# Performance work log

Measured on AMD Instinct MI355X. Metric: run time of the kernel, lower is better.

Reference implementation:

```python
import jax, jax.numpy as jnp
import numpy as np

NEG = -1000000000.0

def setup_inputs() -> dict:
    key = jax.random.key(0)
    kq, kk, kv = jax.random.split(key, 3)
    B, S, D = 4, 4096, 128
    q = jax.random.normal(kq, (B, S, D), dtype=jnp.float32)
    k = jax.random.normal(kk, (B, S, D), dtype=jnp.float32)
    v = jax.random.normal(kv, (B, S, D), dtype=jnp.float32)
    return {"q": q, "k": k, "v": v, "window_size": 128}

def reference(q, k, v, window_size):
    B, S, D = q.shape
    q = q / jnp.sqrt(jnp.asarray(D, q.dtype))
    # banded mask: keep |i-j| <= window_size-1 (tril(w-1) & triu(-(w-1)))
    idx = jnp.arange(S)
    band = jnp.abs(idx[:, None] - idx[None, :]) <= (window_size - 1)  # [S,S]
    scores = jnp.einsum('bqd,bkd->bqk', q, k)
    scores = jnp.where(band[None, :, :], scores, NEG)
    weights = jax.nn.softmax(scores, axis=-1)
    return jnp.einsum('bqk,bkd->bqd', weights, v)
```

## Files before the change

### kernel.cpp

```cpp
#include <hip/hip_runtime.h>

#define S_LEN  4096
#define D_DIM  128
#define MQ     64
#define KT     64
#define NBATCH 4

#define QS_STR 136
#define KS_STR 136
#define VT_STR 72
#define PS_STR 72

typedef __bf16 bf16x8 __attribute__((ext_vector_type(8)));
typedef float  f32x4  __attribute__((ext_vector_type(4)));
typedef unsigned short u16x4 __attribute__((ext_vector_type(4)));
typedef unsigned short u16x8 __attribute__((ext_vector_type(8)));

__device__ __forceinline__ unsigned short f2bf(float f) {
  unsigned int u = __builtin_bit_cast(unsigned int, f);
  u += 0x7fffu + ((u >> 16) & 1u);
  return (unsigned short)(u >> 16);
}

__device__ __forceinline__ bf16x8 ld8(const unsigned short* p) {
  return __builtin_bit_cast(bf16x8, *(const u16x8*)p);
}

__device__ __forceinline__ f32x4 mfma16(bf16x8 a, bf16x8 b, f32x4 c) {
  return __builtin_amdgcn_mfma_f32_16x16x32_bf16(a, b, c, 0, 0, 0);
}

__global__ __launch_bounds__(256)
void swa_fwd(const float* __restrict__ Qg, const float* __restrict__ Kg,
             const float* __restrict__ Vg, float* __restrict__ Og)
{
  __shared__ __align__(16) unsigned short lds_q[MQ * QS_STR];
  __shared__ __align__(16) unsigned short lds_k[KT * KS_STR];
  __shared__ __align__(16) unsigned short lds_vt[D_DIM * VT_STR];
  __shared__ __align__(16) unsigned short lds_p[4 * 16 * PS_STR];

  const int tid  = threadIdx.x;
  const int b    = blockIdx.x >> 6;
  const int q0   = (blockIdx.x & 63) * MQ;
  const size_t base = (size_t)b * S_LEN * D_DIM;

  const int lane = tid & 63;
  const int wv   = tid >> 6;
  const int quad = lane >> 4;
  const int l15  = lane & 15;

  {
    const float qsc = 1.4426950408889634f * 0.08838834764831845f;
    const float* gq = Qg + base + (size_t)q0 * D_DIM;
#pragma unroll
    for (int j = 0; j < 8; ++j) {
      const int f = j * 1024 + tid * 4;
      const int row = f >> 7, col = f & 127;
      const f32x4 x = *(const f32x4*)(gq + f);
      u16x4 y;
#pragma unroll
      for (int e = 0; e < 4; ++e) y[e] = f2bf(x[e] * qsc);
      *(u16x4*)&lds_q[row * QS_STR + col] = y;
    }
  }
  __syncthreads();

  bf16x8 aq[4];
#pragma unroll
  for (int ks = 0; ks < 4; ++ks)
    aq[ks] = ld8(&lds_q[(wv * 16 + l15) * QS_STR + ks * 32 + quad * 8]);

  float mrow[4], lrow[4];
  f32x4 acc[8];
#pragma unroll
  for (int r = 0; r < 4; ++r) { mrow[r] = -3.0e38f; lrow[r] = 0.0f; }
#pragma unroll
  for (int d = 0; d < 8; ++d) acc[d] = (f32x4){0.f, 0.f, 0.f, 0.f};

  for (int t = 0; t < 5; ++t) {
    const int kb = q0 + (t - 2) * KT;
    if (kb < 0 || kb >= S_LEN) continue;
    __syncthreads();

    {
      const float* gk = Kg + base + (size_t)kb * D_DIM;
#pragma unroll
      for (int j = 0; j < 8; ++j) {
        const int f = j * 1024 + tid * 4;
        const int row = f >> 7, col = f & 127;
        const f32x4 x = *(const f32x4*)(gk + f);
        u16x4 y;
#pragma unroll
        for (int e = 0; e < 4; ++e) y[e] = f2bf(x[e]);
        *(u16x4*)&lds_k[row * KS_STR + col] = y;
      }
    }
    {
      const float* gv = Vg + base + (size_t)kb * D_DIM;
      const int d0 = (tid & 31) * 4;
      const int k0 = (tid >> 5) * 8;
      unsigned short vb[4][8];
#pragma unroll
      for (int kk = 0; kk < 8; ++kk) {
        const f32x4 x = *(const f32x4*)(gv + (size_t)(k0 + kk) * D_DIM + d0);
#pragma unroll
        for (int e = 0; e < 4; ++e) vb[e][kk] = f2bf(x[e]);
      }
#pragma unroll
      for (int e = 0; e < 4; ++e) {
        u16x8 y;
#pragma unroll
        for (int kk = 0; kk < 8; ++kk) y[kk] = vb[e][kk];
        *(u16x8*)&lds_vt[(d0 + e) * VT_STR + k0] = y;
      }
    }
    __syncthreads();

    f32x4 sc[4];
#pragma unroll
    for (int cb = 0; cb < 4; ++cb) {
      f32x4 a = (f32x4){0.f, 0.f, 0.f, 0.f};
#pragma unroll
      for (int ks = 0; ks < 4; ++ks) {
        const bf16x8 kf = ld8(&lds_k[(cb * 16 + l15) * KS_STR + ks * 32 + quad * 8]);
        a = mfma16(aq[ks], kf, a);
      }
      sc[cb] = a;
    }

    if (t == 0 || t == 4) {
      const int off = (t - 2) * KT;
#pragma unroll
      for (int cb = 0; cb < 4; ++cb)
#pragma unroll
        for (int r = 0; r < 4; ++r) {
          const int delta = (wv * 16 + quad * 4 + r) - (off + cb * 16 + l15);
          if (delta > 127 || delta < -127) sc[cb][r] = -1.0e30f;
        }
    }

    float tm[4];
#pragma unroll
    for (int r = 0; r < 4; ++r)
      tm[r] = fmaxf(fmaxf(sc[0][r], sc[1][r]), fmaxf(sc[2][r], sc[3][r]));
#pragma unroll
    for (int r = 0; r < 4; ++r) {
      tm[r] = fmaxf(tm[r], __shfl_xor(tm[r], 1, 64));
      tm[r] = fmaxf(tm[r], __shfl_xor(tm[r], 2, 64));
      tm[r] = fmaxf(tm[r], __shfl_xor(tm[r], 4, 64));
      tm[r] = fmaxf(tm[r], __shfl_xor(tm[r], 8, 64));
    }

    float alpha[4], rs[4];
#pragma unroll
    for (int r = 0; r < 4; ++r) {
      const float mn = fmaxf(mrow[r], tm[r]);
      alpha[r] = exp2f(mrow[r] - mn);
      mrow[r] = mn;
    }
#pragma unroll
    for (int cb = 0; cb < 4; ++cb)
#pragma unroll
      for (int r = 0; r < 4; ++r)
        sc[cb][r] = exp2f(sc[cb][r] - mrow[r]);
#pragma unroll
    for (int r = 0; r < 4; ++r) {
      rs[r] = (sc[0][r] + sc[1][r]) + (sc[2][r] + sc[3][r]);
      rs[r] += __shfl_xor(rs[r], 1, 64);
      rs[r] += __shfl_xor(rs[r], 2, 64);
      rs[r] += __shfl_xor(rs[r], 4, 64);
      rs[r] += __shfl_xor(rs[r], 8, 64);
      lrow[r] = lrow[r] * alpha[r] + rs[r];
    }
#pragma unroll
    for (int d = 0; d < 8; ++d)
#pragma unroll
      for (int r = 0; r < 4; ++r) acc[d][r] *= alpha[r];

    unsigned short* pw = &lds_p[wv * 16 * PS_STR];
#pragma unroll
    for (int cb = 0; cb < 4; ++cb)
#pragma unroll
      for (int r = 0; r < 4; ++r)
        pw[(quad * 4 + r) * PS_STR + cb * 16 + l15] = f2bf(sc[cb][r]);

#pragma unroll
    for (int ks2 = 0; ks2 < 2; ++ks2) {
      const bf16x8 pf = ld8(&pw[l15 * PS_STR + ks2 * 32 + quad * 8]);
#pragma unroll
      for (int d = 0; d < 8; ++d) {
        const bf16x8 vf = ld8(&lds_vt[(d * 16 + l15) * VT_STR + ks2 * 32 + quad * 8]);
        acc[d] = mfma16(pf, vf, acc[d]);
      }
    }
  }

  float inv[4];
#pragma unroll
  for (int r = 0; r < 4; ++r) inv[r] = 1.0f / lrow[r];
  float* go = Og + base + (size_t)q0 * D_DIM;
#pragma unroll
  for (int d = 0; d < 8; ++d)
#pragma unroll
    for (int r = 0; r < 4; ++r)
      go[(size_t)(wv * 16 + quad * 4 + r) * D_DIM + d * 16 + l15] = acc[d][r] * inv[r];
}

extern "C" void kernel_launch(void* const* d_in, const int* in_sizes, int n_in,
                              void* d_out, int out_size, void* d_ws, size_t ws_size,
                              hipStream_t stream) {
  const float* q = (const float*)d_in[0];
  const float* k = (const float*)d_in[1];
  const float* v = (const float*)d_in[2];
  float* o = (float*)d_out;
  dim3 grid(NBATCH * (S_LEN / MQ));
  dim3 block(256);
  swa_fwd<<<grid, block, 0, stream>>>(q, k, v, o);
}
```

Measured before the change: 93.33 us.

## Prefetch next K/V tile into registers, skip fully masked blocks, swizzle grid

Global loads of the next K and V tile are issued into registers before the current tile's MFMA and softmax work, then converted and written to LDS after a barrier, so load latency overlaps compute. The loop bounds are computed up front instead of skipping tiles with continue. In edge tiles, column blocks that lie entirely outside the band are skipped. The block index is remapped across batches, and launch bounds now request one block per SM, which trades extra register pressure (three 8-vector register buffers) against possible occupancy loss.

```diff
diff --git a/kernel.cpp b/kernel.cpp
--- a/kernel.cpp
+++ b/kernel.cpp
@@ -30,7 +30,7 @@
   return __builtin_amdgcn_mfma_f32_16x16x32_bf16(a, b, c, 0, 0, 0);
 }
 
-__global__ __launch_bounds__(256)
+__global__ __launch_bounds__(256, 1)
 void swa_fwd(const float* __restrict__ Qg, const float* __restrict__ Kg,
              const float* __restrict__ Vg, float* __restrict__ Og)
 {
@@ -40,8 +40,9 @@
   __shared__ __align__(16) unsigned short lds_p[4 * 16 * PS_STR];
 
   const int tid  = threadIdx.x;
-  const int b    = blockIdx.x >> 6;
-  const int q0   = (blockIdx.x & 63) * MQ;
+  const int g    = (blockIdx.x & 7) * 32 + (blockIdx.x >> 3);
+  const int b    = g >> 6;
+  const int q0   = (g & 63) * MQ;
   const size_t base = (size_t)b * S_LEN * D_DIM;
 
   const int lane = tid & 63;
@@ -49,18 +50,55 @@
   const int quad = lane >> 4;
   const int l15  = lane & 15;
 
+  const int t_lo = (q0 >= 128) ? 0 : (2 - (q0 >> 6));
+  const int t_hi = (4032 - q0 >= 128) ? 4 : (2 + ((4032 - q0) >> 6));
+
+  const int vd0 = (tid & 31) * 4;
+  const int vk0 = (tid >> 5) * 8;
+
+  f32x4 qreg[8], kreg[8], vreg[8];
+  {
+    const float* gq = Qg + base + (size_t)q0 * D_DIM;
+#pragma unroll
+    for (int j = 0; j < 8; ++j) qreg[j] = *(const f32x4*)(gq + j * 1024 + tid * 4);
+  }
+  int kb = q0 + (t_lo - 2) * KT;
+  {
+    const float* gk = Kg + base + (size_t)kb * D_DIM;
+    const float* gv = Vg + base + (size_t)kb * D_DIM;
+#pragma unroll
+    for (int j = 0; j < 8; ++j) kreg[j] = *(const f32x4*)(gk + j * 1024 + tid * 4);
+#pragma unroll
+    for (int kk = 0; kk < 8; ++kk)
+      vreg[kk] = *(const f32x4*)(gv + (size_t)(vk0 + kk) * D_DIM + vd0);
+  }
+
   {
     const float qsc = 1.4426950408889634f * 0.08838834764831845f;
-    const float* gq = Qg + base + (size_t)q0 * D_DIM;
 #pragma unroll
     for (int j = 0; j < 8; ++j) {
       const int f = j * 1024 + tid * 4;
-      const int row = f >> 7, col = f & 127;
-      const f32x4 x = *(const f32x4*)(gq + f);
       u16x4 y;
 #pragma unroll
-      for (int e = 0; e < 4; ++e) y[e] = f2bf(x[e] * qsc);
-      *(u16x4*)&lds_q[row * QS_STR + col] = y;
+      for (int e = 0; e < 4; ++e) y[e] = f2bf(qreg[j][e] * qsc);
+      *(u16x4*)&lds_q[(f >> 7) * QS_STR + (f & 127)] = y;
+    }
+  }
+  {
+#pragma unroll
+    for (int j = 0; j < 8; ++j) {
+      const int f = j * 1024 + tid * 4;
+      u16x4 y;
+#pragma unroll
+      for (int e = 0; e < 4; ++e) y[e] = f2bf(kreg[j][e]);
+      *(u16x4*)&lds_k[(f >> 7) * KS_STR + (f & 127)] = y;
+    }
+#pragma unroll
+    for (int e = 0; e < 4; ++e) {
+      u16x8 y;
+#pragma unroll
+      for (int kk = 0; kk < 8; ++kk) y[kk] = f2bf(vreg[kk][e]);
+      *(u16x8*)&lds_vt[(vd0 + e) * VT_STR + vk0] = y;
     }
   }
   __syncthreads();
@@ -77,48 +115,27 @@
 #pragma unroll
   for (int d = 0; d < 8; ++d) acc[d] = (f32x4){0.f, 0.f, 0.f, 0.f};
 
-  for (int t = 0; t < 5; ++t) {
-    const int kb = q0 + (t - 2) * KT;
-    if (kb < 0 || kb >= S_LEN) continue;
-    __syncthreads();
-
-    {
-      const float* gk = Kg + base + (size_t)kb * D_DIM;
-#pragma unroll
-      for (int j = 0; j < 8; ++j) {
-        const int f = j * 1024 + tid * 4;
-        const int row = f >> 7, col = f & 127;
-        const f32x4 x = *(const f32x4*)(gk + f);
-        u16x4 y;
-#pragma unroll
-        for (int e = 0; e < 4; ++e) y[e] = f2bf(x[e]);
-        *(u16x4*)&lds_k[row * KS_STR + col] = y;
-      }
-    }
-    {
-      const float* gv = Vg + base + (size_t)kb * D_DIM;
-      const int d0 = (tid & 31) * 4;
-      const int k0 = (tid >> 5) * 8;
-      unsigned short vb[4][8];
-#pragma unroll
-      for (int kk = 0; kk < 8; ++kk) {
-        const f32x4 x = *(const f32x4*)(gv + (size_t)(k0 + kk) * D_DIM + d0);
-#pragma unroll
-        for (int e = 0; e < 4; ++e) vb[e][kk] = f2bf(x[e]);
-      }
-#pragma unroll
-      for (int e = 0; e < 4; ++e) {
-        u16x8 y;
-#pragma unroll
-        for (int kk = 0; kk < 8; ++kk) y[kk] = vb[e][kk];
-        *(u16x8*)&lds_vt[(d0 + e) * VT_STR + k0] = y;
-      }
-    }
-    __syncthreads();
-
+  for (int t = t_lo; t <= t_hi; ++t) {
+    if (t < t_hi) {
+      const float* gk = Kg + base + (size_t)(kb + KT) * D_DIM;
+      const float* gv = Vg + base + (size_t)(kb + KT) * D_DIM;
+#pragma unroll
+      for (int j = 0; j < 8; ++j) kreg[j] = *(const f32x4*)(gk + j * 1024 + tid * 4);
+#pragma unroll
+      for (int kk = 0; kk < 8; ++kk)
+        vreg[kk] = *(const f32x4*)(gv + (size_t)(vk0 + kk) * D_DIM + vd0);
+    }
+
+    int cbLo = 0, cbHi = 3;
+    if (t == 0) cbLo = wv;
+    if (t == 4) cbHi = wv;
     f32x4 sc[4];
 #pragma unroll
     for (int cb = 0; cb < 4; ++cb) {
+      if (cb < cbLo || cb > cbHi) {
+        sc[cb] = (f32x4){-1.0e30f, -1.0e30f, -1.0e30f, -1.0e30f};
+        continue;
+      }
       f32x4 a = (f32x4){0.f, 0.f, 0.f, 0.f};
 #pragma unroll
       for (int ks = 0; ks < 4; ++ks) {
@@ -193,6 +210,27 @@
         acc[d] = mfma16(pf, vf, acc[d]);
       }
     }
+
+    __syncthreads();
+    if (t < t_hi) {
+#pragma unroll
+      for (int j = 0; j < 8; ++j) {
+        const int f = j * 1024 + tid * 4;
+        u16x4 y;
+#pragma unroll
+        for (int e = 0; e < 4; ++e) y[e] = f2bf(kreg[j][e]);
+        *(u16x4*)&lds_k[(f >> 7) * KS_STR + (f & 127)] = y;
+      }
+#pragma unroll
+      for (int e = 0; e < 4; ++e) {
+        u16x8 y;
+#pragma unroll
+        for (int kk = 0; kk < 8; ++kk) y[kk] = f2bf(vreg[kk][e]);
+        *(u16x8*)&lds_vt[(vd0 + e) * VT_STR + vk0] = y;
+      }
+    }
+    __syncthreads();
+    kb += KT;
   }
 
   float inv[4];
```

Measured after the change: 91.60 us. About the same (-1.9%).
